# Kernel tuning notes

Measured on AMD Instinct MI355X. Metric: run time of the kernel, lower is better.

## Reference

```python
import jax, jax.numpy as jnp
import numpy as np
import math

B, D, OUT, K = 128, 128, 100000, 4096
T = 0.07
# NOTE: original code reads momentum as params[4], which is -1 (params = [K, T, -1, -1, -1, momentum]).
# We replicate this faithfully: effective momentum = -1.0.
MOMENTUM = -1.0


def setup_inputs() -> dict:
    key = jax.random.key(0)
    k1, k2, k3, k4, k5, k6, k7 = jax.random.split(key, 7)
    stdv = 1.0 / math.sqrt(D / 3)
    return {
        "z1": jax.random.normal(k1, (B, D), dtype=jnp.float32),
        "z2": jax.random.normal(k2, (B, D), dtype=jnp.float32),
        "z3": jax.random.normal(k3, (B, D), dtype=jnp.float32),
        "memory_z2": jax.random.uniform(k4, (OUT, D), dtype=jnp.float32, minval=-stdv, maxval=stdv),
        "memory_z3": jax.random.uniform(k5, (OUT, D), dtype=jnp.float32, minval=-stdv, maxval=stdv),
        "y": jax.random.randint(k6, (B,), 0, OUT, dtype=jnp.int32),
        "idx": jax.random.randint(k7, (B, K + 1), 0, OUT, dtype=jnp.int32),
    }


def _scores(memory, idx, z1, outputSize):
    # gather [B, K+1, D] rows, per-row dot with z1 -> [B, K+1]
    w = jax.lax.stop_gradient(memory)[idx]
    s = jnp.exp(jnp.einsum('bkd,bd->bk', w, z1) / T)[..., None]  # [B, K+1, 1]
    Z = jax.lax.stop_gradient(jnp.mean(s) * outputSize)  # Z_* set on first call
    return s / Z


def _update(memory, y, z):
    pos = memory[y] * MOMENTUM + z * (1.0 - MOMENTUM)  # [B, D]
    pos = pos / jnp.sqrt(jnp.sum(pos * pos, axis=1, keepdims=True))
    return memory.at[y].set(pos)


def reference(z1, z2, z3, memory_z2, memory_z3, y, idx):
    outputSize = memory_z2.shape[0]
    # mimic idx=None path: first column of idx is the positive index y
    idx = idx.at[:, 0].set(y)
    I_z12 = _scores(memory_z2, idx, z1, outputSize)
    I_z13 = _scores(memory_z3, idx, z1, outputSize)
    new_mem2 = _update(memory_z2, y, z2)
    new_mem3 = _update(memory_z3, y, z3)
    return (I_z12, I_z13, new_mem2, new_mem3)
```

## Files before the change

kernel.cpp:

```cpp
#include <hip/hip_runtime.h>

#define BB   128
#define DD   128
#define OUTN 100000
#define KP1  4097
#define TEMP 0.07f

__global__ __launch_bounds__(256) void scores_kernel(
    const float* __restrict__ z1,
    const float* __restrict__ mem2,
    const float* __restrict__ mem3,
    const int*   __restrict__ y,
    const int*   __restrict__ idx,
    float* __restrict__ out,
    float* __restrict__ part)
{
    const int b     = blockIdx.y;
    const int k     = blockIdx.x * blockDim.x + threadIdx.x;
    const bool valid = (k < KP1);
    const int yb    = y[b];

    int j = 0;
    if (valid) j = (k == 0) ? yb : idx[b * KP1 + k];

    const float4* __restrict__ r2 = (const float4*)(mem2 + (size_t)j * DD);
    const float4* __restrict__ r3 = (const float4*)(mem3 + (size_t)j * DD);
    const float4* __restrict__ zz = (const float4*)(z1 + (size_t)b * DD);

    float d2 = 0.f, d3 = 0.f;
    #pragma unroll 8
    for (int c = 0; c < DD / 4; ++c) {
        const float4 zv = zz[c];
        const float4 a2 = r2[c];
        const float4 a3 = r3[c];
        d2 += a2.x * zv.x + a2.y * zv.y + a2.z * zv.z + a2.w * zv.w;
        d3 += a3.x * zv.x + a3.y * zv.y + a3.z * zv.z + a3.w * zv.w;
    }

    float s2 = 0.f, s3 = 0.f;
    if (valid) {
        s2 = expf(d2 * (1.0f / TEMP));
        s3 = expf(d3 * (1.0f / TEMP));
        out[b * KP1 + k]            = s2;
        out[BB * KP1 + b * KP1 + k] = s3;
    }

    #pragma unroll
    for (int off = 32; off > 0; off >>= 1) {
        s2 += __shfl_xor(s2, off);
        s3 += __shfl_xor(s3, off);
    }
    __shared__ float w2[4], w3[4];
    const int wave = threadIdx.x >> 6;
    const int lane = threadIdx.x & 63;
    if (lane == 0) { w2[wave] = s2; w3[wave] = s3; }
    __syncthreads();
    if (threadIdx.x == 0) {
        const float t2 = w2[0] + w2[1] + w2[2] + w2[3];
        const float t3 = w3[0] + w3[1] + w3[2] + w3[3];
        const int slot = (blockIdx.y * gridDim.x + blockIdx.x) & 63;
        atomicAdd(&part[slot],      t2);
        atomicAdd(&part[64 + slot], t3);
    }
}

__global__ __launch_bounds__(256) void scale_kernel(
    float* __restrict__ out, const float* __restrict__ part)
{
    __shared__ float sc[2];
    if (threadIdx.x == 0) {
        float t2 = 0.f, t3 = 0.f;
        for (int i = 0; i < 64; ++i) { t2 += part[i]; t3 += part[64 + i]; }
        sc[0] = (float)((double)(BB * KP1) / ((double)OUTN * (double)t2));
        sc[1] = (float)((double)(BB * KP1) / ((double)OUTN * (double)t3));
    }
    __syncthreads();
    const int i = blockIdx.x * blockDim.x + threadIdx.x;
    if (i >= 2 * BB * KP1) return;
    out[i] *= sc[(i < BB * KP1) ? 0 : 1];
}

__global__ __launch_bounds__(256) void copy_kernel(
    const float4* __restrict__ m2,
    const float4* __restrict__ m3,
    float4* __restrict__ dst)
{
    const int n1 = OUTN * DD / 4;
    const int stride = gridDim.x * blockDim.x;
    for (int i = blockIdx.x * blockDim.x + threadIdx.x; i < 2 * n1; i += stride) {
        dst[i] = (i < n1) ? m2[i] : m3[i - n1];
    }
}

__global__ __launch_bounds__(64) void update_kernel(
    const float* __restrict__ z2,
    const float* __restrict__ z3,
    const float* __restrict__ mem2,
    const float* __restrict__ mem3,
    const int*   __restrict__ y,
    float* __restrict__ out2,
    float* __restrict__ out3)
{
    const int b    = blockIdx.x;
    const int lane = threadIdx.x;
    const int yb   = y[b];

    for (int bp = b + 1; bp < BB; ++bp)
        if (y[bp] == yb) return;

    const float2 m2 = *(const float2*)(mem2 + (size_t)yb * DD + 2 * lane);
    const float2 m3 = *(const float2*)(mem3 + (size_t)yb * DD + 2 * lane);
    const float2 a2 = *(const float2*)(z2 + b * DD + 2 * lane);
    const float2 a3 = *(const float2*)(z3 + b * DD + 2 * lane);

    float2 p2, p3;
    p2.x = 2.f * a2.x - m2.x;  p2.y = 2.f * a2.y - m2.y;
    p3.x = 2.f * a3.x - m3.x;  p3.y = 2.f * a3.y - m3.y;

    float ss2 = p2.x * p2.x + p2.y * p2.y;
    float ss3 = p3.x * p3.x + p3.y * p3.y;
    #pragma unroll
    for (int off = 32; off > 0; off >>= 1) {
        ss2 += __shfl_xor(ss2, off);
        ss3 += __shfl_xor(ss3, off);
    }
    const float inv2 = 1.f / sqrtf(ss2);
    const float inv3 = 1.f / sqrtf(ss3);

    float2 w2, w3;
    w2.x = p2.x * inv2;  w2.y = p2.y * inv2;
    w3.x = p3.x * inv3;  w3.y = p3.y * inv3;
    *(float2*)(out2 + (size_t)yb * DD + 2 * lane) = w2;
    *(float2*)(out3 + (size_t)yb * DD + 2 * lane) = w3;
}

extern "C" void kernel_launch(void* const* d_in, const int* in_sizes, int n_in,
                              void* d_out, int out_size, void* d_ws, size_t ws_size,
                              hipStream_t stream)
{
    const float* z1   = (const float*)d_in[0];
    const float* z2   = (const float*)d_in[1];
    const float* z3   = (const float*)d_in[2];
    const float* mem2 = (const float*)d_in[3];
    const float* mem3 = (const float*)d_in[4];
    const int*   y    = (const int*)d_in[5];
    const int*   idx  = (const int*)d_in[6];
    float*       out  = (float*)d_out;
    float*       part = (float*)d_ws;

    hipMemsetAsync(d_ws, 0, 128 * sizeof(float), stream);

    dim3 gA((KP1 + 255) / 256, BB);
    scores_kernel<<<gA, 256, 0, stream>>>(z1, mem2, mem3, y, idx, out, part);

    const int nScores = 2 * BB * KP1;
    scale_kernel<<<(nScores + 255) / 256, 256, 0, stream>>>(out, part);

    copy_kernel<<<2048, 256, 0, stream>>>((const float4*)mem2, (const float4*)mem3,
                                          (float4*)(out + 2 * BB * KP1));

    update_kernel<<<BB, 64, 0, stream>>>(z2, z3, mem2, mem3, y,
                                         out + 2 * BB * KP1,
                                         out + 2 * BB * KP1 + OUTN * DD);
}
```

Baseline: 307.7 us.

## Fuse memory copy into scores kernel, merge scale and update, cooperative row gather

Each gathered row is now read by eight threads with contiguous 64-byte segments and a shuffle reduction, instead of one thread streaming a whole 512-byte row. The full-memory copy is folded into the scores kernel using nontemporal stores, so the gather and copy traffic share one launch. The scale and update kernels are merged into one launch, cutting the total from four kernels to two. The cost is a more complex kernel with mixed work per block, and scale blocks now index out[] without a bounds check, which relies on the exact block count.

Measured after the change: 272.4 us. 1.13x faster.

```diff
diff --git a/kernel.cpp b/kernel.cpp
--- a/kernel.cpp
+++ b/kernel.cpp
@@ -6,7 +6,14 @@
 #define KP1  4097
 #define TEMP 0.07f
 
-__global__ __launch_bounds__(256) void scores_kernel(
+#define NSB   8320
+#define N1F4  3200000
+#define NF4   6400000
+#define NSCALE_BLK 4097
+
+typedef float vfloat4 __attribute__((ext_vector_type(4)));
+
+__global__ __launch_bounds__(256) void fused_kernel(
     const float* __restrict__ z1,
     const float* __restrict__ mem2,
     const float* __restrict__ mem3,
@@ -15,98 +22,115 @@
     float* __restrict__ out,
     float* __restrict__ part)
 {
-    const int b     = blockIdx.y;
-    const int k     = blockIdx.x * blockDim.x + threadIdx.x;
-    const bool valid = (k < KP1);
-    const int yb    = y[b];
+    const int sb    = blockIdx.x;
+    const int b     = sb & (BB - 1);
+    const int chunk = sb >> 7;
+    const int tid   = threadIdx.x;
+    const int g     = tid & 7;
+    const int grp   = tid >> 3;
 
-    int j = 0;
-    if (valid) j = (k == 0) ? yb : idx[b * KP1 + k];
+    const float4* zz = (const float4*)(z1 + (size_t)b * DD + g * 16);
+    const float4 z0 = zz[0], zv1 = zz[1], zv2 = zz[2], zv3 = zz[3];
 
-    const float4* __restrict__ r2 = (const float4*)(mem2 + (size_t)j * DD);
-    const float4* __restrict__ r3 = (const float4*)(mem3 + (size_t)j * DD);
-    const float4* __restrict__ zz = (const float4*)(z1 + (size_t)b * DD);
+    const int yb = y[b];
 
-    float d2 = 0.f, d3 = 0.f;
-    #pragma unroll 8
-    for (int c = 0; c < DD / 4; ++c) {
-        const float4 zv = zz[c];
-        const float4 a2 = r2[c];
-        const float4 a3 = r3[c];
-        d2 += a2.x * zv.x + a2.y * zv.y + a2.z * zv.z + a2.w * zv.w;
-        d3 += a3.x * zv.x + a3.y * zv.y + a3.z * zv.z + a3.w * zv.w;
+    float acc2 = 0.f, acc3 = 0.f;
+
+    for (int it = 0; it < 2; ++it) {
+        const int k = chunk * 64 + it * 32 + grp;
+        const bool valid = (k < KP1);
+        int j = 0;
+        if (valid) j = (k == 0) ? yb : idx[b * KP1 + k];
+
+        const float4* r2 = (const float4*)(mem2 + (size_t)j * DD + g * 16);
+        const float4* r3 = (const float4*)(mem3 + (size_t)j * DD + g * 16);
+        const float4 a0 = r2[0], a1 = r2[1], a2 = r2[2], a3 = r2[3];
+        const float4 c0 = r3[0], c1 = r3[1], c2 = r3[2], c3 = r3[3];
+
+        float d2 = a0.x*z0.x  + a0.y*z0.y  + a0.z*z0.z  + a0.w*z0.w
+                 + a1.x*zv1.x + a1.y*zv1.y + a1.z*zv1.z + a1.w*zv1.w
+                 + a2.x*zv2.x + a2.y*zv2.y + a2.z*zv2.z + a2.w*zv2.w
+                 + a3.x*zv3.x + a3.y*zv3.y + a3.z*zv3.z + a3.w*zv3.w;
+        float d3 = c0.x*z0.x  + c0.y*z0.y  + c0.z*z0.z  + c0.w*z0.w
+                 + c1.x*zv1.x + c1.y*zv1.y + c1.z*zv1.z + c1.w*zv1.w
+                 + c2.x*zv2.x + c2.y*zv2.y + c2.z*zv2.z + c2.w*zv2.w
+                 + c3.x*zv3.x + c3.y*zv3.y + c3.z*zv3.z + c3.w*zv3.w;
+
+        d2 += __shfl_xor(d2, 1);  d3 += __shfl_xor(d3, 1);
+        d2 += __shfl_xor(d2, 2);  d3 += __shfl_xor(d3, 2);
+        d2 += __shfl_xor(d2, 4);  d3 += __shfl_xor(d3, 4);
+
+        if (valid && g == 0) {
+            const float s2 = expf(d2 * (1.0f / TEMP));
+            const float s3 = expf(d3 * (1.0f / TEMP));
+            out[b * KP1 + k]            = s2;
+            out[BB * KP1 + b * KP1 + k] = s3;
+            acc2 += s2;
+            acc3 += s3;
+        }
     }
 
-    float s2 = 0.f, s3 = 0.f;
-    if (valid) {
-        s2 = expf(d2 * (1.0f / TEMP));
-        s3 = expf(d3 * (1.0f / TEMP));
-        out[b * KP1 + k]            = s2;
-        out[BB * KP1 + b * KP1 + k] = s3;
+    {
+        const vfloat4* m2f = (const vfloat4*)mem2;
+        const vfloat4* m3f = (const vfloat4*)mem3;
+        vfloat4* dstf = (vfloat4*)(out + 2 * BB * KP1);
+        for (int i = sb * 256 + tid; i < NF4; i += NSB * 256) {
+            const vfloat4 v = (i < N1F4) ? m2f[i] : m3f[i - N1F4];
+            __builtin_nontemporal_store(v, dstf + i);
+        }
     }
 
-    #pragma unroll
-    for (int off = 32; off > 0; off >>= 1) {
-        s2 += __shfl_xor(s2, off);
-        s3 += __shfl_xor(s3, off);
-    }
-    __shared__ float w2[4], w3[4];
-    const int wave = threadIdx.x >> 6;
-    const int lane = threadIdx.x & 63;
-    if (lane == 0) { w2[wave] = s2; w3[wave] = s3; }
+    acc2 += __shfl_xor(acc2, 8);   acc3 += __shfl_xor(acc3, 8);
+    acc2 += __shfl_xor(acc2, 16);  acc3 += __shfl_xor(acc3, 16);
+    acc2 += __shfl_xor(acc2, 32);  acc3 += __shfl_xor(acc3, 32);
+
+    __shared__ float w2s[4], w3s[4];
+    const int wave = tid >> 6;
+    const int lane = tid & 63;
+    if (lane == 0) { w2s[wave] = acc2; w3s[wave] = acc3; }
     __syncthreads();
-    if (threadIdx.x == 0) {
-        const float t2 = w2[0] + w2[1] + w2[2] + w2[3];
-        const float t3 = w3[0] + w3[1] + w3[2] + w3[3];
-        const int slot = (blockIdx.y * gridDim.x + blockIdx.x) & 63;
+    if (tid == 0) {
+        const float t2 = w2s[0] + w2s[1] + w2s[2] + w2s[3];
+        const float t3 = w3s[0] + w3s[1] + w3s[2] + w3s[3];
+        const int slot = sb & 63;
         atomicAdd(&part[slot],      t2);
         atomicAdd(&part[64 + slot], t3);
     }
 }
 
-__global__ __launch_bounds__(256) void scale_kernel(
-    float* __restrict__ out, const float* __restrict__ part)
-{
-    __shared__ float sc[2];
-    if (threadIdx.x == 0) {
-        float t2 = 0.f, t3 = 0.f;
-        for (int i = 0; i < 64; ++i) { t2 += part[i]; t3 += part[64 + i]; }
-        sc[0] = (float)((double)(BB * KP1) / ((double)OUTN * (double)t2));
-        sc[1] = (float)((double)(BB * KP1) / ((double)OUTN * (double)t3));
-    }
-    __syncthreads();
-    const int i = blockIdx.x * blockDim.x + threadIdx.x;
-    if (i >= 2 * BB * KP1) return;
-    out[i] *= sc[(i < BB * KP1) ? 0 : 1];
-}
-
-__global__ __launch_bounds__(256) void copy_kernel(
-    const float4* __restrict__ m2,
-    const float4* __restrict__ m3,
-    float4* __restrict__ dst)
-{
-    const int n1 = OUTN * DD / 4;
-    const int stride = gridDim.x * blockDim.x;
-    for (int i = blockIdx.x * blockDim.x + threadIdx.x; i < 2 * n1; i += stride) {
-        dst[i] = (i < n1) ? m2[i] : m3[i - n1];
-    }
-}
-
-__global__ __launch_bounds__(64) void update_kernel(
+__global__ __launch_bounds__(256) void scale_update_kernel(
     const float* __restrict__ z2,
     const float* __restrict__ z3,
     const float* __restrict__ mem2,
     const float* __restrict__ mem3,
     const int*   __restrict__ y,
-    float* __restrict__ out2,
-    float* __restrict__ out3)
+    float* __restrict__ out,
+    const float* __restrict__ part)
 {
-    const int b    = blockIdx.x;
+    if (blockIdx.x < NSCALE_BLK) {
+        __shared__ float sc[2];
+        if (threadIdx.x == 0) {
+            float t2 = 0.f, t3 = 0.f;
+            for (int i = 0; i < 64; ++i) { t2 += part[i]; t3 += part[64 + i]; }
+            sc[0] = (float)((double)(BB * KP1) / ((double)OUTN * (double)t2));
+            sc[1] = (float)((double)(BB * KP1) / ((double)OUTN * (double)t3));
+        }
+        __syncthreads();
+        const int i = blockIdx.x * 256 + threadIdx.x;
+        out[i] *= sc[(i < BB * KP1) ? 0 : 1];
+        return;
+    }
+
+    const int b    = blockIdx.x - NSCALE_BLK;
     const int lane = threadIdx.x;
-    const int yb   = y[b];
+    if (lane >= 64) return;
+    const int yb = y[b];
 
     for (int bp = b + 1; bp < BB; ++bp)
         if (y[bp] == yb) return;
+
+    float* out2 = out + 2 * BB * KP1;
+    float* out3 = out2 + OUTN * DD;
 
     const float2 m2 = *(const float2*)(mem2 + (size_t)yb * DD + 2 * lane);
     const float2 m3 = *(const float2*)(mem3 + (size_t)yb * DD + 2 * lane);
@@ -150,16 +174,8 @@
 
     hipMemsetAsync(d_ws, 0, 128 * sizeof(float), stream);
 
-    dim3 gA((KP1 + 255) / 256, BB);
-    scores_kernel<<<gA, 256, 0, stream>>>(z1, mem2, mem3, y, idx, out, part);
+    fused_kernel<<<NSB, 256, 0, stream>>>(z1, mem2, mem3, y, idx, out, part);
 
-    const int nScores = 2 * BB * KP1;
-    scale_kernel<<<(nScores + 255) / 256, 256, 0, stream>>>(out, part);
-
-    copy_kernel<<<2048, 256, 0, stream>>>((const float4*)mem2, (const float4*)mem3,
-                                          (float4*)(out + 2 * BB * KP1));
-
-    update_kernel<<<BB, 64, 0, stream>>>(z2, z3, mem2, mem3, y,
-                                         out + 2 * BB * KP1,
-                                         out + 2 * BB * KP1 + OUTN * DD);
+    scale_update_kernel<<<NSCALE_BLK + BB, 256, 0, stream>>>(
+        z2, z3, mem2, mem3, y, out, part);
 }
```

## Replace gathered dot products with dense memory×z1 GEMM then gather scores

Applied to the files above, without the earlier changes.

Instead of gathering 2×128×4097 memory rows (about 537MB of random reads), the new code computes the full dense product of each memory bank with z1ᵀ (100000×128×128) using a shared-memory-tiled FP32 GEMM. A gather kernel then reads the needed scalar scores. The memory copy is fused into the GEMM load when workspace is large enough, and the scale and copy kernels are merged. This trades the redundant gather bandwidth for about 3.3 GFLOP of FP32 compute per bank plus a 102MB intermediate score matrix.

Measured after the change: 344.5 us. 1.12x slower.

```diff
diff --git a/kernel.cpp b/kernel.cpp
--- a/kernel.cpp
+++ b/kernel.cpp
@@ -6,89 +6,170 @@
 #define KP1  4097
 #define TEMP 0.07f
 
-__global__ __launch_bounds__(256) void scores_kernel(
-    const float* __restrict__ z1,
-    const float* __restrict__ mem2,
-    const float* __restrict__ mem3,
-    const int*   __restrict__ y,
-    const int*   __restrict__ idx,
-    float* __restrict__ out,
+#define JT     128
+#define NJT    782
+#define SCORES (2 * BB * KP1)
+#define NROW   (OUTN * DD)
+#define N1F4   (NROW / 4)
+#define NF4    (2 * N1F4)
+#define NSCALE_BLK 4097
+#define NCPB   4096
+
+typedef float vfloat4 __attribute__((ext_vector_type(4)));
+
+__global__ __launch_bounds__(256) void prep_kernel(
+    const float* __restrict__ z1, float* __restrict__ z1t,
     float* __restrict__ part)
 {
-    const int b     = blockIdx.y;
-    const int k     = blockIdx.x * blockDim.x + threadIdx.x;
-    const bool valid = (k < KP1);
-    const int yb    = y[b];
-
-    int j = 0;
-    if (valid) j = (k == 0) ? yb : idx[b * KP1 + k];
-
-    const float4* __restrict__ r2 = (const float4*)(mem2 + (size_t)j * DD);
-    const float4* __restrict__ r3 = (const float4*)(mem3 + (size_t)j * DD);
-    const float4* __restrict__ zz = (const float4*)(z1 + (size_t)b * DD);
-
-    float d2 = 0.f, d3 = 0.f;
-    #pragma unroll 8
-    for (int c = 0; c < DD / 4; ++c) {
-        const float4 zv = zz[c];
-        const float4 a2 = r2[c];
-        const float4 a3 = r3[c];
-        d2 += a2.x * zv.x + a2.y * zv.y + a2.z * zv.z + a2.w * zv.w;
-        d3 += a3.x * zv.x + a3.y * zv.y + a3.z * zv.z + a3.w * zv.w;
-    }
-
-    float s2 = 0.f, s3 = 0.f;
-    if (valid) {
-        s2 = expf(d2 * (1.0f / TEMP));
-        s3 = expf(d3 * (1.0f / TEMP));
-        out[b * KP1 + k]            = s2;
-        out[BB * KP1 + b * KP1 + k] = s3;
-    }
-
+    const int bid = blockIdx.x;
+    if (bid == 64) {
+        if (threadIdx.x < 128) part[threadIdx.x] = 0.f;
+        return;
+    }
+    const int e = bid * 256 + threadIdx.x;
+    const int d = e >> 7, b = e & 127;
+    z1t[e] = z1[b * DD + d];
+}
+
+__global__ __launch_bounds__(256, 2) void gemm_kernel(
+    const float* __restrict__ mem2, const float* __restrict__ mem3,
+    const float* __restrict__ z1t,
+    float* __restrict__ s2, float* __restrict__ s3,
+    float* __restrict__ cpy2, float* __restrict__ cpy3, int do_copy)
+{
+    __shared__ vfloat4 tile[128 * 32];
+    const int t  = threadIdx.x;
+    const int tx = t & 15;
+    const int ty = t >> 4;
+    const long jt = (long)blockIdx.x * JT;
+    const vfloat4* z1tf = (const vfloat4*)z1t;
+
+    for (int m = 0; m < 2; ++m) {
+        const vfloat4* mem = (const vfloat4*)(m ? mem3 : mem2);
+        float* sd = m ? s3 : s2;
+        vfloat4* cd = (vfloat4*)(m ? cpy3 : cpy2);
+        if (m) __syncthreads();
+
+        #pragma unroll
+        for (int i = 0; i < 16; ++i) {
+            const int e = i * 256 + t;
+            const int j = e >> 5, c = e & 31;
+            const long gj = jt + j;
+            vfloat4 v = {0.f, 0.f, 0.f, 0.f};
+            if (gj < OUTN) v = mem[gj * 32 + c];
+            tile[j * 32 + (c ^ (j >> 3))] = v;
+            if (do_copy && gj < OUTN)
+                __builtin_nontemporal_store(v, cd + gj * 32 + c);
+        }
+        __syncthreads();
+
+        float acc[8][8];
+        #pragma unroll
+        for (int a = 0; a < 8; ++a)
+            #pragma unroll
+            for (int bbi = 0; bbi < 8; ++bbi) acc[a][bbi] = 0.f;
+
+        for (int d4 = 0; d4 < 32; ++d4) {
+            vfloat4 zA[4], zB[4];
+            #pragma unroll
+            for (int q = 0; q < 4; ++q) {
+                zA[q] = z1tf[(d4 * 4 + q) * 32 + tx];
+                zB[q] = z1tf[(d4 * 4 + q) * 32 + 16 + tx];
+            }
+            #pragma unroll
+            for (int h = 0; h < 2; ++h) {
+                vfloat4 mj[4];
+                #pragma unroll
+                for (int r = 0; r < 4; ++r) {
+                    const int j = ty * 8 + h * 4 + r;
+                    mj[r] = tile[j * 32 + (d4 ^ ty)];
+                }
+                #pragma unroll
+                for (int q = 0; q < 4; ++q)
+                    #pragma unroll
+                    for (int r = 0; r < 4; ++r) {
+                        const float mv = mj[r][q];
+                        #pragma unroll
+                        for (int bbi = 0; bbi < 4; ++bbi) {
+                            acc[h * 4 + r][bbi]     += mv * zA[q][bbi];
+                            acc[h * 4 + r][4 + bbi] += mv * zB[q][bbi];
+                        }
+                    }
+            }
+        }
+
+        #pragma unroll
+        for (int jj = 0; jj < 8; ++jj) {
+            const long gj = jt + ty * 8 + jj;
+            if (gj < OUTN) {
+                vfloat4 o0 = {acc[jj][0], acc[jj][1], acc[jj][2], acc[jj][3]};
+                vfloat4 o1 = {acc[jj][4], acc[jj][5], acc[jj][6], acc[jj][7]};
+                *(vfloat4*)(sd + gj * DD + tx * 4)      = o0;
+                *(vfloat4*)(sd + gj * DD + 64 + tx * 4) = o1;
+            }
+        }
+    }
+}
+
+__global__ __launch_bounds__(256) void gather_kernel(
+    const float* __restrict__ S2, const float* __restrict__ S3,
+    const int* __restrict__ y, const int* __restrict__ idx,
+    float* __restrict__ out, float* __restrict__ part)
+{
+    const int b = blockIdx.y;
+    const int k = blockIdx.x * 256 + threadIdx.x;
+    float s2v = 0.f, s3v = 0.f;
+    if (k < KP1) {
+        const int j = (k == 0) ? y[b] : idx[b * KP1 + k];
+        s2v = expf(S2[(size_t)j * DD + b] * (1.0f / TEMP));
+        s3v = expf(S3[(size_t)j * DD + b] * (1.0f / TEMP));
+        out[b * KP1 + k]            = s2v;
+        out[BB * KP1 + b * KP1 + k] = s3v;
+    }
     #pragma unroll
     for (int off = 32; off > 0; off >>= 1) {
-        s2 += __shfl_xor(s2, off);
-        s3 += __shfl_xor(s3, off);
-    }
-    __shared__ float w2[4], w3[4];
+        s2v += __shfl_xor(s2v, off);
+        s3v += __shfl_xor(s3v, off);
+    }
+    __shared__ float w2s[4], w3s[4];
     const int wave = threadIdx.x >> 6;
     const int lane = threadIdx.x & 63;
-    if (lane == 0) { w2[wave] = s2; w3[wave] = s3; }
+    if (lane == 0) { w2s[wave] = s2v; w3s[wave] = s3v; }
     __syncthreads();
     if (threadIdx.x == 0) {
-        const float t2 = w2[0] + w2[1] + w2[2] + w2[3];
-        const float t3 = w3[0] + w3[1] + w3[2] + w3[3];
+        const float t2 = w2s[0] + w2s[1] + w2s[2] + w2s[3];
+        const float t3 = w3s[0] + w3s[1] + w3s[2] + w3s[3];
         const int slot = (blockIdx.y * gridDim.x + blockIdx.x) & 63;
         atomicAdd(&part[slot],      t2);
         atomicAdd(&part[64 + slot], t3);
     }
 }
 
-__global__ __launch_bounds__(256) void scale_kernel(
-    float* __restrict__ out, const float* __restrict__ part)
-{
-    __shared__ float sc[2];
-    if (threadIdx.x == 0) {
-        float t2 = 0.f, t3 = 0.f;
-        for (int i = 0; i < 64; ++i) { t2 += part[i]; t3 += part[64 + i]; }
-        sc[0] = (float)((double)(BB * KP1) / ((double)OUTN * (double)t2));
-        sc[1] = (float)((double)(BB * KP1) / ((double)OUTN * (double)t3));
-    }
-    __syncthreads();
-    const int i = blockIdx.x * blockDim.x + threadIdx.x;
-    if (i >= 2 * BB * KP1) return;
-    out[i] *= sc[(i < BB * KP1) ? 0 : 1];
-}
-
-__global__ __launch_bounds__(256) void copy_kernel(
-    const float4* __restrict__ m2,
-    const float4* __restrict__ m3,
-    float4* __restrict__ dst)
-{
-    const int n1 = OUTN * DD / 4;
-    const int stride = gridDim.x * blockDim.x;
-    for (int i = blockIdx.x * blockDim.x + threadIdx.x; i < 2 * n1; i += stride) {
-        dst[i] = (i < n1) ? m2[i] : m3[i - n1];
+__global__ __launch_bounds__(256) void finalize_kernel(
+    const float* __restrict__ mem2, const float* __restrict__ mem3,
+    float* __restrict__ out, const float* __restrict__ part, int do_copy)
+{
+    if (blockIdx.x < NSCALE_BLK) {
+        __shared__ float sc[2];
+        if (threadIdx.x == 0) {
+            float t2 = 0.f, t3 = 0.f;
+            for (int i = 0; i < 64; ++i) { t2 += part[i]; t3 += part[64 + i]; }
+            sc[0] = (float)((double)(BB * KP1) / ((double)OUTN * (double)t2));
+            sc[1] = (float)((double)(BB * KP1) / ((double)OUTN * (double)t3));
+        }
+        __syncthreads();
+        const int i = blockIdx.x * 256 + threadIdx.x;
+        out[i] *= sc[(i < BB * KP1) ? 0 : 1];
+        return;
+    }
+    if (!do_copy) return;
+    const vfloat4* m2f = (const vfloat4*)mem2;
+    const vfloat4* m3f = (const vfloat4*)mem3;
+    vfloat4* dstf = (vfloat4*)(out + SCORES);
+    for (int i = (blockIdx.x - NSCALE_BLK) * 256 + threadIdx.x; i < NF4;
+         i += NCPB * 256) {
+        const vfloat4 v = (i < N1F4) ? m2f[i] : m3f[i - N1F4];
+        __builtin_nontemporal_store(v, dstf + i);
     }
 }
 
@@ -148,18 +229,24 @@
     float*       out  = (float*)d_out;
     float*       part = (float*)d_ws;
 
-    hipMemsetAsync(d_ws, 0, 128 * sizeof(float), stream);
-
-    dim3 gA((KP1 + 255) / 256, BB);
-    scores_kernel<<<gA, 256, 0, stream>>>(z1, mem2, mem3, y, idx, out, part);
-
-    const int nScores = 2 * BB * KP1;
-    scale_kernel<<<(nScores + 255) / 256, 256, 0, stream>>>(out, part);
-
-    copy_kernel<<<2048, 256, 0, stream>>>((const float4*)mem2, (const float4*)mem3,
-                                          (float4*)(out + 2 * BB * KP1));
+    const bool big = ws_size >= ((size_t)2 * NROW + 256) * sizeof(float);
+    float* S2 = big ? (part + 256) : (out + SCORES);
+    float* S3 = S2 + NROW;
+    float* z1t = out;
+
+    prep_kernel<<<65, 256, 0, stream>>>(z1, z1t, part);
+
+    gemm_kernel<<<NJT, 256, 0, stream>>>(mem2, mem3, z1t, S2, S3,
+                                         out + SCORES, out + SCORES + NROW,
+                                         big ? 1 : 0);
+
+    dim3 gg(17, BB);
+    gather_kernel<<<gg, 256, 0, stream>>>(S2, S3, y, idx, out, part);
+
+    finalize_kernel<<<NSCALE_BLK + (big ? 0 : NCPB), 256, 0, stream>>>(
+        mem2, mem3, out, part, big ? 0 : 1);
 
     update_kernel<<<BB, 64, 0, stream>>>(z2, z3, mem2, mem3, y,
-                                         out + 2 * BB * KP1,
-                                         out + 2 * BB * KP1 + OUTN * DD);
-}
+                                         out + SCORES,
+                                         out + SCORES + NROW);
+}
```
